# Optimization experiments

Measured on AMD Instinct MI355X. Metric: run time of the kernel, lower is better.

## Reference

```python
import jax, jax.numpy as jnp
import numpy as np

POOLED = 7          # square pooled grid (grid_width == grid_height required by torch_combined_meshgrid)
NUM_LEVELS = 6      # len_feature_maps; level = clamp(floor(5 + log2(sqrt(w*h))), 0, 5)


def _bilinear_sample(fm, gx, gy):
    """fm: [C, D, D]; gx, gy: [N, G, G] normalized coords in [0,1].
    Faithful to getWeightedSum_ofFourFmapPoints: floor/ceil corner points with
    proportion weights; coord dim 0 (x) indexes fmap rows, dim 1 (y) indexes cols.
    Returns [N, C, G, G]."""
    D = fm.shape[-1]
    ux = gx * (D - 1)
    uy = gy * (D - 1)
    x0 = jnp.floor(ux); x1 = jnp.ceil(ux)
    y0 = jnp.floor(uy); y1 = jnp.ceil(uy)
    ddx = jnp.where(x1 - x0 == 0, 1.0, x1 - x0)
    ddy = jnp.where(y1 - y0 == 0, 1.0, y1 - y0)
    px0 = 1.0 - (ux - x0) / ddx   # proportion_to_take_from_start_x
    px1 = 1.0 - px0
    py0 = 1.0 - (uy - y0) / ddy
    py1 = 1.0 - py0
    ix0 = x0.astype(jnp.int32); ix1 = x1.astype(jnp.int32)
    iy0 = y0.astype(jnp.int32); iy1 = y1.astype(jnp.int32)
    # advanced indexing: fm[:, idx, idx] -> [C, N, G, G]
    tl = fm[:, ix0, iy0]
    tr = fm[:, ix1, iy0]
    bl = fm[:, ix0, iy1]
    br = fm[:, ix1, iy1]
    w_tl = (px0 * py0)[None]
    w_tr = (px1 * py0)[None]
    w_bl = (px0 * py1)[None]
    w_br = (px1 * py1)[None]
    pooled = w_tl * tl + w_tr * tr + w_bl * bl + w_br * br  # [C, N, G, G]
    return jnp.moveaxis(pooled, 0, 1)                        # [N, C, G, G]


def setup_inputs() -> dict:
    key = jax.random.key(0)
    N, C = 2000, 256
    dims = [38, 19, 10, 5, 3, 1]
    kw, kh, kx, ky, *kf = jax.random.split(key, 4 + len(dims))
    w = jax.random.uniform(kw, (N, 1), minval=0.02, maxval=0.98)
    h = jax.random.uniform(kh, (N, 1), minval=0.02, maxval=0.98)
    x1 = jax.random.uniform(kx, (N, 1)) * (1.0 - w)
    y1 = jax.random.uniform(ky, (N, 1)) * (1.0 - h)
    boxes = jnp.concatenate([x1, y1, x1 + w, y1 + h], axis=1)  # x1 y1 x2 y2 in [0,1]
    out = {"boxes": boxes}
    for i, (d, k) in enumerate(zip(dims, kf)):
        out[f"fmap{i}"] = jax.random.normal(k, (1, C, d, d), dtype=jnp.float32)
    return out


def reference(boxes, fmap0, fmap1, fmap2, fmap3, fmap4, fmap5):
    fmaps = [fmap0, fmap1, fmap2, fmap3, fmap4, fmap5]
    N = boxes.shape[0]
    C = fmap0.shape[1]
    G = POOLED
    x1, y1, x2, y2 = boxes[:, 0:1], boxes[:, 1:2], boxes[:, 2:3], boxes[:, 3:4]
    # FPN-style level index: floor(5 + log2(sqrt(w*h))), clamped (constant w.r.t. grad)
    avg = jnp.sqrt((x2 - x1) * (y2 - y1))
    lvl = jnp.clip(jnp.floor((NUM_LEVELS - 1.0) + jnp.log2(avg)), 0, NUM_LEVELS - 1)
    lvl = jax.lax.stop_gradient(lvl.astype(jnp.int32).reshape(-1))  # [N]
    # bilinear interpolation grid: grid[n,i,j] = (x1 + i*dx/(G-1), y1 + j*dy/(G-1)), clamped
    t = jnp.arange(G, dtype=boxes.dtype)
    denom = max(1.0, G - 1.0)
    xr = jnp.clip(x1 + t[None, :] * (x2 - x1) / denom, 0.0, 1.0)  # [N, G]
    yr = jnp.clip(y1 + t[None, :] * (y2 - y1) / denom, 0.0, 1.0)  # [N, G]
    gx = jnp.broadcast_to(xr[:, :, None], (N, G, G))
    gy = jnp.broadcast_to(yr[:, None, :], (N, G, G))
    out = jnp.zeros((N, C, G, G), dtype=fmap0.dtype)
    for l, f in enumerate(fmaps):
        fm = f[0]  # [C, D, D] (single image; one fmap selected per box)
        if fm.shape[-1] == 1:
            # original returns fmap[:, :, 0:1, 0:1]; broadcast the constant to the grid
            pooled = jnp.broadcast_to(fm[None, :, :1, :1], (N, C, G, G))
        else:
            pooled = _bilinear_sample(fm, gx, gy)
        mask = (lvl == l).astype(fmap0.dtype)[:, None, None, None]
        out = out + mask * pooled
    return out
```

## Files before the change

kernel.cpp:

```cpp
#include <hip/hip_runtime.h>

#define G 7
#define CCH 256
#define NLVL 6

__device__ __constant__ int kD[NLVL]  = {38, 19, 10, 5, 3, 1};
__device__ __constant__ int kD2[NLVL] = {1444, 361, 100, 25, 9, 1};
__device__ __constant__ int kBaseT[NLVL + 1] = {0, 369664, 462080, 487680, 494080, 496384, 496640};

#define FMT_TOTAL 496640

__global__ __launch_bounds__(256) void transpose_fmaps(
    const float* __restrict__ f0, const float* __restrict__ f1,
    const float* __restrict__ f2, const float* __restrict__ f3,
    const float* __restrict__ f4, const float* __restrict__ f5,
    float* __restrict__ fmT)
{
    int o = blockIdx.x * blockDim.x + threadIdx.x;
    if (o >= FMT_TOTAL) return;
    int l = 0;
#pragma unroll
    for (int k = 1; k < NLVL; ++k) l += (o >= kBaseT[k]);
    int rel = o - kBaseT[l];
    int p = rel >> 8;
    int c = rel & 255;
    const float* f;
    switch (l) {
        case 0: f = f0; break;
        case 1: f = f1; break;
        case 2: f = f2; break;
        case 3: f = f3; break;
        case 4: f = f4; break;
        default: f = f5; break;
    }
    fmT[o] = f[c * kD2[l] + p];
}

__global__ __launch_bounds__(256) void roialign_main(
    const float* __restrict__ boxes, const float* __restrict__ fmT,
    float* __restrict__ out)
{
    __shared__ float sOut[CCH * 49];

    int n = blockIdx.x;
    int tid = threadIdx.x;

    float bx1 = boxes[n * 4 + 0];
    float by1 = boxes[n * 4 + 1];
    float bx2 = boxes[n * 4 + 2];
    float by2 = boxes[n * 4 + 3];
    float w = bx2 - bx1;
    float h = by2 - by1;
    float avg = sqrtf(w * h);
    float lf = floorf((float)(NLVL - 1) + log2f(avg));
    lf = fminf(fmaxf(lf, 0.0f), (float)(NLVL - 1));
    int lvl = __builtin_amdgcn_readfirstlane((int)lf);
    int D    = kD[lvl];
    int base = kBaseT[lvl];
    float Dm1 = (float)(D - 1);
    int Dm1i = D - 1;
    int Drow = D << 8;
    float w6 = w * (1.0f / 6.0f);
    float h6 = h * (1.0f / 6.0f);
    int baset = base + tid;

    float* row = sOut + tid * 49;

#pragma unroll
    for (int g = 0; g < 49; ++g) {
        const int i = g / 7;
        const int j = g - 7 * i;
        float xr = fminf(fmaxf(fmaf((float)i, w6, bx1), 0.0f), 1.0f);
        float yr = fminf(fmaxf(fmaf((float)j, h6, by1), 0.0f), 1.0f);
        float ux = xr * Dm1;
        float uy = yr * Dm1;
        float xf = floorf(ux);
        float yf = floorf(uy);
        float fx = ux - xf;
        float fy = uy - yf;
        int ix0 = (int)xf;
        int iy0 = (int)yf;
        int o00 = baset + ((ix0 * D + iy0) << 8);
        int dxo = (ix0 < Dm1i) ? Drow : 0;
        int dyo = (iy0 < Dm1i) ? 256 : 0;
        float a00 = fmT[o00];
        float a10 = fmT[o00 + dxo];
        float a01 = fmT[o00 + dyo];
        float a11 = fmT[o00 + dxo + dyo];
        float px0 = 1.0f - fx, py0 = 1.0f - fy;
        float vx0 = px0 * a00 + fx * a10;
        float vx1 = px0 * a01 + fx * a11;
        row[g] = py0 * vx0 + fy * vx1;
    }

    asm volatile("s_waitcnt lgkmcnt(0)" ::: "memory");
    __builtin_amdgcn_sched_barrier(0);

    int wv_id = tid >> 6;
    int lane = tid & 63;
    const float4* s4 = (const float4*)sOut + wv_id * 784;
    float4* out4 = (float4*)(out + (size_t)n * (CCH * G * G)) + wv_id * 784;
#pragma unroll
    for (int k = 0; k < 12; ++k) {
        out4[k * 64 + lane] = s4[k * 64 + lane];
    }
    if (lane < 16) out4[768 + lane] = s4[768 + lane];
}

__global__ __launch_bounds__(256) void roialign_fallback(
    const float* __restrict__ boxes,
    const float* __restrict__ f0, const float* __restrict__ f1,
    const float* __restrict__ f2, const float* __restrict__ f3,
    const float* __restrict__ f4, const float* __restrict__ f5,
    float* __restrict__ out, int total4)
{
    int t = blockIdx.x * blockDim.x + threadIdx.x;
    if (t >= total4) return;
    const int perN = CCH * G * G;
    int idx = t * 4;
    int n = idx / perN;
    int rem = idx - n * perN;
    float bx1 = boxes[n * 4 + 0], by1 = boxes[n * 4 + 1];
    float bx2 = boxes[n * 4 + 2], by2 = boxes[n * 4 + 3];
    float w = bx2 - bx1, h = by2 - by1;
    float avg = sqrtf(w * h);
    float lf = floorf((float)(NLVL - 1) + log2f(avg));
    lf = fminf(fmaxf(lf, 0.0f), (float)(NLVL - 1));
    int lvl = (int)lf;
    const float* fm;
    switch (lvl) {
        case 0: fm = f0; break;
        case 1: fm = f1; break;
        case 2: fm = f2; break;
        case 3: fm = f3; break;
        case 4: fm = f4; break;
        default: fm = f5; break;
    }
    int D = kD[lvl];
    float Dm1 = (float)(D - 1);
    float4 res;
    float* rp = &res.x;
#pragma unroll
    for (int k = 0; k < 4; ++k) {
        int e = rem + k;
        int j = e % G;
        int iq = e / G;
        int i = iq % G;
        int c = iq / G;
        float xr = fminf(fmaxf(bx1 + ((float)i * w) / 6.0f, 0.0f), 1.0f);
        float yr = fminf(fmaxf(by1 + ((float)j * h) / 6.0f, 0.0f), 1.0f);
        float ux = xr * Dm1, uy = yr * Dm1;
        float x0 = floorf(ux), y0 = floorf(uy);
        int ix0 = (int)x0, iy0 = (int)y0;
        float fx = ux - x0, fy = uy - y0;
        int ix1 = min(ix0 + 1, D - 1), iy1 = min(iy0 + 1, D - 1);
        const float* p = fm + c * D * D;
        float v00 = p[ix0 * D + iy0], v10 = p[ix1 * D + iy0];
        float v01 = p[ix0 * D + iy1], v11 = p[ix1 * D + iy1];
        float px0 = 1.0f - fx, py0 = 1.0f - fy;
        rp[k] = px0 * py0 * v00 + fx * py0 * v10 + px0 * fy * v01 + fx * fy * v11;
    }
    reinterpret_cast<float4*>(out)[t] = res;
}

extern "C" void kernel_launch(void* const* d_in, const int* in_sizes, int n_in,
                              void* d_out, int out_size, void* d_ws, size_t ws_size,
                              hipStream_t stream) {
    const float* boxes = (const float*)d_in[0];
    const float* f0 = (const float*)d_in[1];
    const float* f1 = (const float*)d_in[2];
    const float* f2 = (const float*)d_in[3];
    const float* f3 = (const float*)d_in[4];
    const float* f4 = (const float*)d_in[5];
    const float* f5 = (const float*)d_in[6];
    float* out = (float*)d_out;
    int N = in_sizes[0] / 4;

    if (ws_size >= (size_t)FMT_TOTAL * sizeof(float)) {
        float* fmT = (float*)d_ws;
        transpose_fmaps<<<(FMT_TOTAL + 255) / 256, 256, 0, stream>>>(
            f0, f1, f2, f3, f4, f5, fmT);
        roialign_main<<<N, 256, 0, stream>>>(boxes, fmT, out);
    } else {
        int total4 = out_size / 4;
        roialign_fallback<<<(total4 + 255) / 256, 256, 0, stream>>>(
            boxes, f0, f1, f2, f3, f4, f5, out, total4);
    }
}
```

Measured before the change: 32.04 us.

## Shrink LDS staging to per-wave 16-channel slabs and split rows across lanes

Replaces the 50KB per-block shared output buffer with a small per-wave slab covering 16 channels at a time. Each lane handles one channel and a subset of grid rows, and the wave flushes each slab to global memory before moving on. The smaller LDS footprint is meant to allow more resident blocks per CU and to interleave the global stores with the gathers. In exchange, each wave now has four load/store phases, the x-interpolation terms are computed once per row and reused across columns, and the gathers become less coalesced because only 16 consecutive channels are read per address.

```diff
diff --git a/kernel.cpp b/kernel.cpp
--- a/kernel.cpp
+++ b/kernel.cpp
@@ -40,10 +40,14 @@
     const float* __restrict__ boxes, const float* __restrict__ fmT,
     float* __restrict__ out)
 {
-    __shared__ float sOut[CCH * 49];
+    __shared__ float slab[4][784];
 
     int n = blockIdx.x;
     int tid = threadIdx.x;
+    int wv = tid >> 6;
+    int lane = tid & 63;
+    int cl = lane & 15;
+    int q  = lane >> 4;
 
     float bx1 = boxes[n * 4 + 0];
     float by1 = boxes[n * 4 + 1];
@@ -60,51 +64,58 @@
     float Dm1 = (float)(D - 1);
     int Dm1i = D - 1;
     int Drow = D << 8;
-    float w6 = w * (1.0f / 6.0f);
-    float h6 = h * (1.0f / 6.0f);
-    int baset = base + tid;
-
-    float* row = sOut + tid * 49;
-
-#pragma unroll
-    for (int g = 0; g < 49; ++g) {
-        const int i = g / 7;
-        const int j = g - 7 * i;
-        float xr = fminf(fmaxf(fmaf((float)i, w6, bx1), 0.0f), 1.0f);
-        float yr = fminf(fmaxf(fmaf((float)j, h6, by1), 0.0f), 1.0f);
-        float ux = xr * Dm1;
-        float uy = yr * Dm1;
-        float xf = floorf(ux);
-        float yf = floorf(uy);
-        float fx = ux - xf;
-        float fy = uy - yf;
-        int ix0 = (int)xf;
-        int iy0 = (int)yf;
-        int o00 = baset + ((ix0 * D + iy0) << 8);
-        int dxo = (ix0 < Dm1i) ? Drow : 0;
-        int dyo = (iy0 < Dm1i) ? 256 : 0;
-        float a00 = fmT[o00];
-        float a10 = fmT[o00 + dxo];
-        float a01 = fmT[o00 + dyo];
-        float a11 = fmT[o00 + dxo + dyo];
-        float px0 = 1.0f - fx, py0 = 1.0f - fy;
-        float vx0 = px0 * a00 + fx * a10;
-        float vx1 = px0 * a01 + fx * a11;
-        row[g] = py0 * vx0 + fy * vx1;
-    }
-
-    asm volatile("s_waitcnt lgkmcnt(0)" ::: "memory");
-    __builtin_amdgcn_sched_barrier(0);
-
-    int wv_id = tid >> 6;
-    int lane = tid & 63;
-    const float4* s4 = (const float4*)sOut + wv_id * 784;
-    float4* out4 = (float4*)(out + (size_t)n * (CCH * G * G)) + wv_id * 784;
-#pragma unroll
-    for (int k = 0; k < 12; ++k) {
-        out4[k * 64 + lane] = s4[k * 64 + lane];
-    }
-    if (lane < 16) out4[768 + lane] = s4[768 + lane];
+
+    float* ms = slab[wv];
+    size_t boxBase = (size_t)n * (CCH * G * G);
+
+#pragma unroll
+    for (int hh = 0; hh < 4; ++hh) {
+        int c = wv * 64 + hh * 16 + cl;
+        int bt = base + c;
+
+#pragma unroll
+        for (int r = 0; r < 2; ++r) {
+            int i = q + 4 * r;
+            if (r == 0 || q < 3) {
+                float xr = fminf(fmaxf(bx1 + ((float)i * w) / 6.0f, 0.0f), 1.0f);
+                float ux = xr * Dm1;
+                float xf = floorf(ux);
+                float fx = ux - xf;
+                int ix0 = (int)xf;
+                int oxa = ix0 * Drow;
+                int oxb = oxa + ((ix0 < Dm1i) ? Drow : 0);
+                float px0 = 1.0f - fx;
+                int rb = cl * 49 + i * 7;
+#pragma unroll
+                for (int j = 0; j < 7; ++j) {
+                    float yr = fminf(fmaxf(by1 + ((float)j * h) / 6.0f, 0.0f), 1.0f);
+                    float uy = yr * Dm1;
+                    float yf = floorf(uy);
+                    float fy = uy - yf;
+                    int iy0 = (int)yf;
+                    int oya = iy0 << 8;
+                    int oyb = oya + ((iy0 < Dm1i) ? 256 : 0);
+                    float a00 = fmT[bt + oxa + oya];
+                    float a10 = fmT[bt + oxb + oya];
+                    float a01 = fmT[bt + oxa + oyb];
+                    float a11 = fmT[bt + oxb + oyb];
+                    float vx0 = px0 * a00 + fx * a10;
+                    float vx1 = px0 * a01 + fx * a11;
+                    ms[rb + j] = (1.0f - fy) * vx0 + fy * vx1;
+                }
+            }
+        }
+
+        asm volatile("s_waitcnt lgkmcnt(0)" ::: "memory");
+        __builtin_amdgcn_sched_barrier(0);
+
+        const float4* s4 = (const float4*)ms;
+        float4* out4 = (float4*)(out + boxBase) + (wv * 784 + hh * 196);
+        out4[lane]       = s4[lane];
+        out4[64 + lane]  = s4[64 + lane];
+        out4[128 + lane] = s4[128 + lane];
+        if (lane < 4) out4[192 + lane] = s4[192 + lane];
+    }
 }
 
 __global__ __launch_bounds__(256) void roialign_fallback(
```

After: 34.39 us. 1.07x slower.
